# Optimization experiments

Measured on AMD Instinct MI355X. Metric: run time of the kernel, lower is better.

## Reference

```python
import jax, jax.numpy as jnp
import numpy as np

MARGIN = 0.2
ENCODER_STRIDE = 320


def setup_inputs() -> dict:
    key = jax.random.key(0)
    k1, k2, k3, k4 = jax.random.split(key, 4)
    B, D, T, NC = 8, 512, 2048, 4096
    student_features = jax.random.normal(k1, (B, D, T), dtype=jnp.float32)
    codebook = jax.random.normal(k2, (NC, D), dtype=jnp.float32)
    teacher_codes = jax.random.randint(k3, (B, T), 0, NC, dtype=jnp.int64)
    lengths = jax.random.randint(k4, (B,), 0, T * ENCODER_STRIDE, dtype=jnp.int64)
    return {
        "student_features": student_features,
        "teacher_codes": teacher_codes,
        "codebook": codebook,
        "lengths": lengths,
    }


def reference(student_features, teacher_codes, codebook, lengths):
    B, D, T = student_features.shape
    # frame-level valid mask: (B, T)
    frame_lengths = lengths // ENCODER_STRIDE
    mask = (jnp.arange(T)[None, :] < frame_lengths[:, None]).astype(student_features.dtype)

    # (B*T, D) flattened student vectors
    z = jnp.transpose(student_features, (0, 2, 1)).reshape(-1, D)

    # Euclidean cdist via ||z||^2 + ||c||^2 - 2 z c^T (matmul form, like torch.cdist)
    sq = (
        jnp.sum(z * z, axis=-1, keepdims=True)
        + jnp.sum(codebook * codebook, axis=-1)[None, :]
        - 2.0 * jnp.einsum("nd,cd->nc", z, codebook)
    )
    dists = jnp.sqrt(jnp.maximum(sq, 1e-12))  # (B*T, num_codes)

    teacher_flat = teacher_codes.reshape(-1)
    rows = jnp.arange(teacher_flat.shape[0])
    pos_dist = dists[rows, teacher_flat]
    # exclude the target code, then min over codebook
    dists_for_neg = dists.at[rows, teacher_flat].set(jnp.inf)
    neg_dist = jnp.min(dists_for_neg, axis=1)

    triplet = jax.nn.relu(pos_dist.reshape(B, T) - neg_dist.reshape(B, T) + MARGIN)
    loss = jnp.sum(triplet * mask) / (jnp.sum(mask) + 1e-8)
    return loss
```

## Files before the change

### kernel.cpp

```cpp
#include <hip/hip_runtime.h>
#include <hip/hip_bf16.h>

typedef __bf16 bf16x8 __attribute__((ext_vector_type(8)));
typedef float f32x4 __attribute__((ext_vector_type(4)));
typedef int v8i __attribute__((ext_vector_type(8)));

#define NB 8
#define ND 512
#define NT 2048
#define NCODES 4096
#define NM (NB * NT)
#define MARGIN_F 0.2f
#define ENC_STRIDE 320


static __device__ inline unsigned short f2bf(float v) {
    __hip_bfloat16 h = __float2bfloat16(v);
    return __builtin_bit_cast(unsigned short, h);
}

static __device__ inline void async_copy16(const void* g, void* l) {
    __builtin_amdgcn_global_load_lds(
        (const __attribute__((address_space(1))) unsigned int*)g,
        (__attribute__((address_space(3))) unsigned int*)l, 16, 0, 0);
}

__global__ void prep_fused(const float* __restrict__ sf, const float* __restrict__ cb,
                           unsigned char* __restrict__ Zq, unsigned short* __restrict__ Zrm,
                           unsigned char* __restrict__ Cq, float* __restrict__ cnorm) {
    __shared__ float tile[128][65];
    __shared__ float redc[4][16];
    const int tid = threadIdx.x;
    const int wave = tid >> 6, lane = tid & 63, l15 = lane & 15, kq = lane >> 4;

    if (blockIdx.x < 1024) {
        const int bx = blockIdx.x;
        const int t0 = (bx & 31) * 64;
        const int d0 = ((bx >> 5) & 3) * 128;
        const int b = bx >> 7;
        const float* src = sf + (size_t)b * ND * NT;
#pragma unroll
        for (int it = 0; it < 8; it++) {
            int idx = it * 256 + tid;
            int d = idx >> 4, t4 = (idx & 15) * 4;
            float4 v = *(const float4*)(src + (size_t)(d0 + d) * NT + t0 + t4);
            tile[d][t4] = v.x; tile[d][t4 + 1] = v.y; tile[d][t4 + 2] = v.z; tile[d][t4 + 3] = v.w;
        }
        __syncthreads();
        const int m0 = b * NT + t0;
        {
            const int trow = wave * 16 + l15;
            unsigned char q[32];
#pragma unroll
            for (int j = 0; j < 32; j += 2) {
                float a = tile[kq * 32 + j][trow];
                float c = tile[kq * 32 + j + 1][trow];
                int p = __builtin_amdgcn_cvt_pk_fp8_f32(a, c, 0, false);
                q[j] = (unsigned char)(p & 0xFF);
                q[j + 1] = (unsigned char)((p >> 8) & 0xFF);
            }
            const int M_ = m0 >> 7, rg = ((m0 >> 4) & 7) + wave, K_ = d0 >> 7;
            char* base = (char*)Zq + ((size_t)((M_ * 4 + K_) * 8 + rg)) * 2048;
            *(uint4*)(base + lane * 16) = *(uint4*)&q[0];
            *(uint4*)(base + 1024 + lane * 16) = *(uint4*)&q[16];
        }
        {
            int t = tid >> 2;
#pragma unroll
            for (int it = 0; it < 8; it++) {
                int d = (tid & 3) * 4 + it * 16;
                ushort4 o;
                o.x = f2bf(tile[d][t]); o.y = f2bf(tile[d + 1][t]);
                o.z = f2bf(tile[d + 2][t]); o.w = f2bf(tile[d + 3][t]);
                *(ushort4*)(Zrm + (size_t)(m0 + t) * ND + d0 + d) = o;
            }
        }
    } else {
        const int r0 = (blockIdx.x - 1024) * 16;
        const int row = r0 + l15;
        const int K_ = wave;
        const float* src = cb + (size_t)row * ND + K_ * 128 + kq * 32;
        unsigned char q[32];
        float s = 0.0f;
#pragma unroll
        for (int j4 = 0; j4 < 8; j4++) {
            float4 v = *(const float4*)(src + j4 * 4);
            s += v.x * v.x + v.y * v.y + v.z * v.z + v.w * v.w;
            int p0 = __builtin_amdgcn_cvt_pk_fp8_f32(v.x, v.y, 0, false);
            int p1 = __builtin_amdgcn_cvt_pk_fp8_f32(v.z, v.w, 0, false);
            q[j4 * 4 + 0] = (unsigned char)(p0 & 0xFF);
            q[j4 * 4 + 1] = (unsigned char)((p0 >> 8) & 0xFF);
            q[j4 * 4 + 2] = (unsigned char)(p1 & 0xFF);
            q[j4 * 4 + 3] = (unsigned char)((p1 >> 8) & 0xFF);
        }
        const int N_ = r0 >> 7, rg = (r0 >> 4) & 7;
        char* base = (char*)Cq + ((size_t)((N_ * 4 + K_) * 8 + rg)) * 2048;
        *(uint4*)(base + lane * 16) = *(uint4*)&q[0];
        *(uint4*)(base + 1024 + lane * 16) = *(uint4*)&q[16];
        s += __shfl_xor(s, 16);
        s += __shfl_xor(s, 32);
        if (lane < 16) redc[wave][l15] = s;
        __syncthreads();
        if (tid < 16) cnorm[r0 + tid] = redc[0][tid] + redc[1][tid] + redc[2][tid] + redc[3][tid];
    }
}

__global__ __launch_bounds__(256, 2) void triplet_main(
    const unsigned char* __restrict__ Zq, const unsigned char* __restrict__ Cq,
    const float* __restrict__ cnorm, const int* __restrict__ teacher,
    unsigned int* __restrict__ minq) {
    __shared__ __align__(16) unsigned char As[16384];
    __shared__ __align__(16) unsigned char Bs[16384];

    const int M_ = blockIdx.x;
    const int nq = blockIdx.y;
    const int m0 = M_ * 128;
    const int tid = threadIdx.x;
    const int wave = tid >> 6, lane = tid & 63;
    const int wr = wave >> 1, wc = wave & 1;
    const int l15 = lane & 15, quad = lane >> 4;

    unsigned int minu[4][4];
    int tch[4][4];
#pragma unroll
    for (int mi = 0; mi < 4; mi++)
#pragma unroll
        for (int r = 0; r < 4; r++) {
            minu[mi][r] = 0xFFFFFFFFu;
            tch[mi][r] = teacher[m0 + wr * 64 + mi * 16 + quad * 4 + r];
        }

    const char* gA0 = (const char*)Zq + (size_t)M_ * 4 * 16384 + wave * 4096 + lane * 16;
    char* lA = (char*)As + wave * 4096;
    char* lB = (char*)Bs + wave * 4096;

    for (int nt = 0; nt < 4; nt++) {
        const int N_ = nq * 4 + nt;
        const int n0 = N_ * 128;
        const char* gA = gA0;
        const char* gB = (const char*)Cq + (size_t)N_ * 4 * 16384 + wave * 4096 + lane * 16;
        f32x4 acc[4][4] = {};

        for (int kt = 0; kt < 4; kt++) {
#pragma unroll
            for (int i = 0; i < 4; i++) {
                async_copy16(gA + i * 1024, lA + i * 1024);
                async_copy16(gB + i * 1024, lB + i * 1024);
            }
            gA += 16384; gB += 16384;
            __syncthreads();

            v8i av[4], bv[4];
#pragma unroll
            for (int mi = 0; mi < 4; mi++) {
                int rg = wr * 4 + mi;
                union { uint4 q[2]; v8i v; } u;
                u.q[0] = *(const uint4*)(As + rg * 2048 + lane * 16);
                u.q[1] = *(const uint4*)(As + rg * 2048 + 1024 + lane * 16);
                av[mi] = u.v;
            }
#pragma unroll
            for (int ni = 0; ni < 4; ni++) {
                int rg = wc * 4 + ni;
                union { uint4 q[2]; v8i v; } u;
                u.q[0] = *(const uint4*)(Bs + rg * 2048 + lane * 16);
                u.q[1] = *(const uint4*)(Bs + rg * 2048 + 1024 + lane * 16);
                bv[ni] = u.v;
            }
#pragma unroll
            for (int mi = 0; mi < 4; mi++)
#pragma unroll
                for (int ni = 0; ni < 4; ni++)
                    acc[mi][ni] = __builtin_amdgcn_mfma_scale_f32_16x16x128_f8f6f4(
                        av[mi], bv[ni], acc[mi][ni], 0, 0,
                        0, 0x7F7F7F7F, 0, 0x7F7F7F7F);
            __syncthreads();
        }

        float cn[4]; int col[4];
#pragma unroll
        for (int ni = 0; ni < 4; ni++) {
            col[ni] = n0 + wc * 64 + ni * 16 + l15;
            cn[ni] = cnorm[col[ni]];
        }
#pragma unroll
        for (int mi = 0; mi < 4; mi++)
#pragma unroll
            for (int r = 0; r < 4; r++) {
                int t = tch[mi][r];
#pragma unroll
                for (int ni = 0; ni < 4; ni++) {
                    float val = fmaxf(fmaf(-2.0f, acc[mi][ni][r], cn[ni]), 0.0f);
                    unsigned int u = (__builtin_bit_cast(unsigned int, val) & 0xFFFFF000u)
                                     | (unsigned int)col[ni];
                    u = (col[ni] == t) ? 0xFFFFFFFFu : u;
                    minu[mi][r] = min(minu[mi][r], u);
                }
            }
    }

    const int slot = nq * 2 + wc;
#pragma unroll
    for (int mi = 0; mi < 4; mi++)
#pragma unroll
        for (int r = 0; r < 4; r++) {
            unsigned int u = minu[mi][r];
#pragma unroll
            for (int off = 1; off < 16; off <<= 1) u = min(u, (unsigned int)__shfl_xor((int)u, off));
            if (l15 == 0) {
                int m = m0 + wr * 64 + mi * 16 + quad * 4 + r;
                minq[(size_t)slot * NM + m] = u;
            }
        }
}

__global__ void refine(const unsigned short* __restrict__ Zrm, const float* __restrict__ cb,
                       const unsigned int* __restrict__ minq, const int* __restrict__ teacher,
                       const int* __restrict__ lengths, float* __restrict__ blocksums) {
    const int tid = threadIdx.x, wave = tid >> 6, lane = tid & 63;
    const int m = blockIdx.x * 4 + wave;
    unsigned int u = minq[(size_t)(lane & 15) * NM + m];
    u = min(u, (unsigned int)__shfl_xor((int)u, 1));
    u = min(u, (unsigned int)__shfl_xor((int)u, 2));
    u = min(u, (unsigned int)__shfl_xor((int)u, 4));
    u = min(u, (unsigned int)__shfl_xor((int)u, 8));
    const int ng = (int)(u & 0xFFFu);
    const int tch = teacher[m];
    bf16x8 z8 = *(const bf16x8*)(Zrm + (size_t)m * ND + lane * 8);
    const float* cn_ = cb + (size_t)ng * ND + lane * 8;
    const float* ct_ = cb + (size_t)tch * ND + lane * 8;
    float an = 0.0f, at = 0.0f;
#pragma unroll
    for (int i = 0; i < 2; i++) {
        float4 vn = *(const float4*)(cn_ + i * 4);
        float4 vt = *(const float4*)(ct_ + i * 4);
        float z0 = (float)z8[i * 4 + 0], z1 = (float)z8[i * 4 + 1];
        float z2 = (float)z8[i * 4 + 2], z3 = (float)z8[i * 4 + 3];
        float d;
        d = z0 - vn.x; an += d * d;  d = z0 - vt.x; at += d * d;
        d = z1 - vn.y; an += d * d;  d = z1 - vt.y; at += d * d;
        d = z2 - vn.z; an += d * d;  d = z2 - vt.z; at += d * d;
        d = z3 - vn.w; an += d * d;  d = z3 - vt.w; at += d * d;
    }
#pragma unroll
    for (int off = 1; off < 64; off <<= 1) {
        an += __shfl_xor(an, off);
        at += __shfl_xor(at, off);
    }
    __shared__ float red[4];
    if (lane == 0) {
        float negd = sqrtf(fmaxf(an, 1e-12f));
        float posd = sqrtf(fmaxf(at, 1e-12f));
        float tri = fmaxf(posd - negd + MARGIN_F, 0.0f);
        int t = m & (NT - 1);
        int b = m >> 11;
        int flen = lengths[b] / ENC_STRIDE;
        red[wave] = (t < flen) ? tri : 0.0f;
    }
    __syncthreads();
    if (tid == 0) blocksums[blockIdx.x] = red[0] + red[1] + red[2] + red[3];
}

__global__ void finalize(const float* __restrict__ blocksums, const int* __restrict__ lengths,
                         float* __restrict__ out) {
    int tid = threadIdx.x;
    float s = 0.0f;
#pragma unroll
    for (int i = 0; i < 16; i++) s += blocksums[tid + i * 256];
#pragma unroll
    for (int off = 1; off < 64; off <<= 1) s += __shfl_xor(s, off);
    __shared__ float red[4];
    int lane = tid & 63, w = tid >> 6;
    if (lane == 0) red[w] = s;
    __syncthreads();
    if (tid == 0) {
        float cnt = 0.0f;
        for (int b = 0; b < NB; b++) cnt += (float)(lengths[b] / ENC_STRIDE);
        out[0] = (red[0] + red[1] + red[2] + red[3]) / (cnt + 1e-8f);
    }
}

extern "C" void kernel_launch(void* const* d_in, const int* in_sizes, int n_in,
                              void* d_out, int out_size, void* d_ws, size_t ws_size,
                              hipStream_t stream) {
    const float* sf = (const float*)d_in[0];
    const int* teacher = (const int*)d_in[1];
    const float* cb = (const float*)d_in[2];
    const int* lengths = (const int*)d_in[3];

    char* ws = (char*)d_ws;
    unsigned char* Zq = (unsigned char*)(ws);
    unsigned char* Cq = (unsigned char*)(ws + 8388608);
    unsigned short* Zrm = (unsigned short*)(ws + 10485760);
    float* cnorm = (float*)(ws + 27262976);
    unsigned int* minq = (unsigned int*)(ws + 27279360);
    float* blocksums = (float*)(ws + 28327936);

    prep_fused<<<1280, 256, 0, stream>>>(sf, cb, Zq, Zrm, Cq, cnorm);
    triplet_main<<<dim3(128, 8), 256, 0, stream>>>(Zq, Cq, cnorm, teacher, minq);
    refine<<<NM / 4, 256, 0, stream>>>(Zrm, cb, minq, teacher, lengths, blocksums);
    finalize<<<1, 256, 0, stream>>>(blocksums, lengths, (float*)d_out);
}
```

Before: 147.1 us.

## Double-buffer LDS tiles in triplet_main with flattened prefetch loop

Doubles the A and B shared-memory buffers and flattens the nt/kt loops into 16 steps. Each step first prefetches the next K-tile with async global-to-LDS copies into the other buffer, then runs MFMAs on the current one, so global load latency overlaps with compute. It also drops one of the two barriers per step. The cost is twice the LDS per block, which could limit occupancy, and the epilogue min-reduction now sits inside the pipelined loop.

```diff
diff --git a/kernel.cpp b/kernel.cpp
--- a/kernel.cpp
+++ b/kernel.cpp
@@ -109,8 +109,8 @@
     const unsigned char* __restrict__ Zq, const unsigned char* __restrict__ Cq,
     const float* __restrict__ cnorm, const int* __restrict__ teacher,
     unsigned int* __restrict__ minq) {
-    __shared__ __align__(16) unsigned char As[16384];
-    __shared__ __align__(16) unsigned char Bs[16384];
+    __shared__ __align__(16) unsigned char As[2][16384];
+    __shared__ __align__(16) unsigned char Bs[2][16384];
 
     const int M_ = blockIdx.x;
     const int nq = blockIdx.y;
@@ -130,73 +130,96 @@
             tch[mi][r] = teacher[m0 + wr * 64 + mi * 16 + quad * 4 + r];
         }
 
-    const char* gA0 = (const char*)Zq + (size_t)M_ * 4 * 16384 + wave * 4096 + lane * 16;
-    char* lA = (char*)As + wave * 4096;
-    char* lB = (char*)Bs + wave * 4096;
-
-    for (int nt = 0; nt < 4; nt++) {
-        const int N_ = nq * 4 + nt;
-        const int n0 = N_ * 128;
-        const char* gA = gA0;
-        const char* gB = (const char*)Cq + (size_t)N_ * 4 * 16384 + wave * 4096 + lane * 16;
-        f32x4 acc[4][4] = {};
-
-        for (int kt = 0; kt < 4; kt++) {
+    const char* gA0 = (const char*)Zq + (size_t)M_ * 65536 + wave * 4096 + lane * 16;
+    const char* gB0 = (const char*)Cq + (size_t)(nq * 4) * 65536 + wave * 4096 + lane * 16;
+
+    {
+        char* lA = (char*)As[0] + wave * 4096;
+        char* lB = (char*)Bs[0] + wave * 4096;
+#pragma unroll
+        for (int i = 0; i < 4; i++) {
+            async_copy16(gA0 + i * 1024, lA + i * 1024);
+            async_copy16(gB0 + i * 1024, lB + i * 1024);
+        }
+    }
+
+    f32x4 acc[4][4];
+
+    for (int s = 0; s < 16; s++) {
+        __syncthreads();
+
+        if (s < 15) {
+            int sn = s + 1;
+            int ktn = sn & 3, ntn = sn >> 2;
+            const char* gA = gA0 + ktn * 16384;
+            const char* gB = gB0 + (size_t)ntn * 65536 + ktn * 16384;
+            char* lA = (char*)As[sn & 1] + wave * 4096;
+            char* lB = (char*)Bs[sn & 1] + wave * 4096;
 #pragma unroll
             for (int i = 0; i < 4; i++) {
                 async_copy16(gA + i * 1024, lA + i * 1024);
                 async_copy16(gB + i * 1024, lB + i * 1024);
             }
-            gA += 16384; gB += 16384;
-            __syncthreads();
-
-            v8i av[4], bv[4];
-#pragma unroll
-            for (int mi = 0; mi < 4; mi++) {
-                int rg = wr * 4 + mi;
-                union { uint4 q[2]; v8i v; } u;
-                u.q[0] = *(const uint4*)(As + rg * 2048 + lane * 16);
-                u.q[1] = *(const uint4*)(As + rg * 2048 + 1024 + lane * 16);
-                av[mi] = u.v;
-            }
+        }
+
+        if ((s & 3) == 0) {
+#pragma unroll
+            for (int mi = 0; mi < 4; mi++)
+#pragma unroll
+                for (int ni = 0; ni < 4; ni++) acc[mi][ni] = (f32x4){0.f, 0.f, 0.f, 0.f};
+        }
+
+        const unsigned char* bufA = As[s & 1];
+        const unsigned char* bufB = Bs[s & 1];
+        v8i av[4], bv[4];
+#pragma unroll
+        for (int mi = 0; mi < 4; mi++) {
+            int rg = wr * 4 + mi;
+            union { uint4 q[2]; v8i v; } u;
+            u.q[0] = *(const uint4*)(bufA + rg * 2048 + lane * 16);
+            u.q[1] = *(const uint4*)(bufA + rg * 2048 + 1024 + lane * 16);
+            av[mi] = u.v;
+        }
+#pragma unroll
+        for (int ni = 0; ni < 4; ni++) {
+            int rg = wc * 4 + ni;
+            union { uint4 q[2]; v8i v; } u;
+            u.q[0] = *(const uint4*)(bufB + rg * 2048 + lane * 16);
+            u.q[1] = *(const uint4*)(bufB + rg * 2048 + 1024 + lane * 16);
+            bv[ni] = u.v;
+        }
+#pragma unroll
+        for (int mi = 0; mi < 4; mi++)
+#pragma unroll
+            for (int ni = 0; ni < 4; ni++)
+                acc[mi][ni] = __builtin_amdgcn_mfma_scale_f32_16x16x128_f8f6f4(
+                    av[mi], bv[ni], acc[mi][ni], 0, 0,
+                    0, 0x7F7F7F7F, 0, 0x7F7F7F7F);
+
+        if ((s & 3) == 3) {
+            const int nt = s >> 2;
+            const int n0 = (nq * 4 + nt) * 128;
+            float cn[4]; int col[4];
 #pragma unroll
             for (int ni = 0; ni < 4; ni++) {
-                int rg = wc * 4 + ni;
-                union { uint4 q[2]; v8i v; } u;
-                u.q[0] = *(const uint4*)(Bs + rg * 2048 + lane * 16);
-                u.q[1] = *(const uint4*)(Bs + rg * 2048 + 1024 + lane * 16);
-                bv[ni] = u.v;
+                col[ni] = n0 + wc * 64 + ni * 16 + l15;
+                cn[ni] = cnorm[col[ni]];
             }
 #pragma unroll
             for (int mi = 0; mi < 4; mi++)
 #pragma unroll
-                for (int ni = 0; ni < 4; ni++)
-                    acc[mi][ni] = __builtin_amdgcn_mfma_scale_f32_16x16x128_f8f6f4(
-                        av[mi], bv[ni], acc[mi][ni], 0, 0,
-                        0, 0x7F7F7F7F, 0, 0x7F7F7F7F);
-            __syncthreads();
-        }
-
-        float cn[4]; int col[4];
-#pragma unroll
-        for (int ni = 0; ni < 4; ni++) {
-            col[ni] = n0 + wc * 64 + ni * 16 + l15;
-            cn[ni] = cnorm[col[ni]];
-        }
-#pragma unroll
-        for (int mi = 0; mi < 4; mi++)
-#pragma unroll
-            for (int r = 0; r < 4; r++) {
-                int t = tch[mi][r];
-#pragma unroll
-                for (int ni = 0; ni < 4; ni++) {
-                    float val = fmaxf(fmaf(-2.0f, acc[mi][ni][r], cn[ni]), 0.0f);
-                    unsigned int u = (__builtin_bit_cast(unsigned int, val) & 0xFFFFF000u)
-                                     | (unsigned int)col[ni];
-                    u = (col[ni] == t) ? 0xFFFFFFFFu : u;
-                    minu[mi][r] = min(minu[mi][r], u);
+                for (int r = 0; r < 4; r++) {
+                    int t = tch[mi][r];
+#pragma unroll
+                    for (int ni = 0; ni < 4; ni++) {
+                        float val = fmaxf(fmaf(-2.0f, acc[mi][ni][r], cn[ni]), 0.0f);
+                        unsigned int u = (__builtin_bit_cast(unsigned int, val) & 0xFFFFF000u)
+                                         | (unsigned int)col[ni];
+                        u = (col[ni] == t) ? 0xFFFFFFFFu : u;
+                        minu[mi][r] = min(minu[mi][r], u);
+                    }
                 }
-            }
+        }
     }
 
     const int slot = nq * 2 + wc;
```

New measurement: 148.1 us. Within noise of the previous version (+0.7%).

## Keep full A tile resident in LDS and stream B fragments directly from global

Applied to the files above, without the earlier changes.

The whole 128x512 fp8 Z tile (64KB) is loaded into LDS once per block rather than once per N tile and K step. The codebook operand is now read straight from global memory into registers in two halves per K step. This removes the per-iteration __syncthreads barriers and the redundant re-staging of A. In exchange each block needs 64KB of LDS, which may cut occupancy below the launch bound of 2 blocks per CU. B loads also go through global/L2 latency with little software pipelining.

```diff
diff --git a/kernel.cpp b/kernel.cpp
--- a/kernel.cpp
+++ b/kernel.cpp
@@ -109,8 +109,7 @@
     const unsigned char* __restrict__ Zq, const unsigned char* __restrict__ Cq,
     const float* __restrict__ cnorm, const int* __restrict__ teacher,
     unsigned int* __restrict__ minq) {
-    __shared__ __align__(16) unsigned char As[16384];
-    __shared__ __align__(16) unsigned char Bs[16384];
+    __shared__ __align__(16) unsigned char As[65536];
 
     const int M_ = blockIdx.x;
     const int nq = blockIdx.y;
@@ -120,6 +119,13 @@
     const int wr = wave >> 1, wc = wave & 1;
     const int l15 = lane & 15, quad = lane >> 4;
 
+    {
+        const char* gA = (const char*)Zq + (size_t)M_ * 65536 + wave * 16384 + lane * 16;
+        char* lA = (char*)As + wave * 16384;
+#pragma unroll
+        for (int i = 0; i < 16; i++) async_copy16(gA + i * 1024, lA + i * 1024);
+    }
+
     unsigned int minu[4][4];
     int tch[4][4];
 #pragma unroll
@@ -129,52 +135,50 @@
             minu[mi][r] = 0xFFFFFFFFu;
             tch[mi][r] = teacher[m0 + wr * 64 + mi * 16 + quad * 4 + r];
         }
-
-    const char* gA0 = (const char*)Zq + (size_t)M_ * 4 * 16384 + wave * 4096 + lane * 16;
-    char* lA = (char*)As + wave * 4096;
-    char* lB = (char*)Bs + wave * 4096;
+    __syncthreads();
 
     for (int nt = 0; nt < 4; nt++) {
         const int N_ = nq * 4 + nt;
         const int n0 = N_ * 128;
-        const char* gA = gA0;
-        const char* gB = (const char*)Cq + (size_t)N_ * 4 * 16384 + wave * 4096 + lane * 16;
+        const char* gB = (const char*)Cq + (size_t)N_ * 65536 + (wc * 4) * 2048 + lane * 16;
         f32x4 acc[4][4] = {};
 
         for (int kt = 0; kt < 4; kt++) {
-#pragma unroll
-            for (int i = 0; i < 4; i++) {
-                async_copy16(gA + i * 1024, lA + i * 1024);
-                async_copy16(gB + i * 1024, lB + i * 1024);
-            }
-            gA += 16384; gB += 16384;
-            __syncthreads();
-
-            v8i av[4], bv[4];
+            const char* gBk = gB + kt * 16384;
+            const unsigned char* aB = As + (kt * 8 + wr * 4) * 2048 + lane * 16;
+
+            union { uint4 q[2]; v8i v; } b0, b1;
+            b0.q[0] = *(const uint4*)(gBk);
+            b0.q[1] = *(const uint4*)(gBk + 1024);
+            b1.q[0] = *(const uint4*)(gBk + 2048);
+            b1.q[1] = *(const uint4*)(gBk + 3072);
+
+            v8i av[4];
 #pragma unroll
             for (int mi = 0; mi < 4; mi++) {
-                int rg = wr * 4 + mi;
                 union { uint4 q[2]; v8i v; } u;
-                u.q[0] = *(const uint4*)(As + rg * 2048 + lane * 16);
-                u.q[1] = *(const uint4*)(As + rg * 2048 + 1024 + lane * 16);
+                u.q[0] = *(const uint4*)(aB + mi * 2048);
+                u.q[1] = *(const uint4*)(aB + mi * 2048 + 1024);
                 av[mi] = u.v;
             }
 #pragma unroll
-            for (int ni = 0; ni < 4; ni++) {
-                int rg = wc * 4 + ni;
-                union { uint4 q[2]; v8i v; } u;
-                u.q[0] = *(const uint4*)(Bs + rg * 2048 + lane * 16);
-                u.q[1] = *(const uint4*)(Bs + rg * 2048 + 1024 + lane * 16);
-                bv[ni] = u.v;
-            }
-#pragma unroll
-            for (int mi = 0; mi < 4; mi++)
-#pragma unroll
-                for (int ni = 0; ni < 4; ni++)
-                    acc[mi][ni] = __builtin_amdgcn_mfma_scale_f32_16x16x128_f8f6f4(
-                        av[mi], bv[ni], acc[mi][ni], 0, 0,
-                        0, 0x7F7F7F7F, 0, 0x7F7F7F7F);
-            __syncthreads();
+            for (int mi = 0; mi < 4; mi++) {
+                acc[mi][0] = __builtin_amdgcn_mfma_scale_f32_16x16x128_f8f6f4(
+                    av[mi], b0.v, acc[mi][0], 0, 0, 0, 0x7F7F7F7F, 0, 0x7F7F7F7F);
+                acc[mi][1] = __builtin_amdgcn_mfma_scale_f32_16x16x128_f8f6f4(
+                    av[mi], b1.v, acc[mi][1], 0, 0, 0, 0x7F7F7F7F, 0, 0x7F7F7F7F);
+            }
+            b0.q[0] = *(const uint4*)(gBk + 4096);
+            b0.q[1] = *(const uint4*)(gBk + 5120);
+            b1.q[0] = *(const uint4*)(gBk + 6144);
+            b1.q[1] = *(const uint4*)(gBk + 7168);
+#pragma unroll
+            for (int mi = 0; mi < 4; mi++) {
+                acc[mi][2] = __builtin_amdgcn_mfma_scale_f32_16x16x128_f8f6f4(
+                    av[mi], b0.v, acc[mi][2], 0, 0, 0, 0x7F7F7F7F, 0, 0x7F7F7F7F);
+                acc[mi][3] = __builtin_amdgcn_mfma_scale_f32_16x16x128_f8f6f4(
+                    av[mi], b1.v, acc[mi][3], 0, 0, 0, 0x7F7F7F7F, 0, 0x7F7F7F7F);
+            }
         }
 
         float cn[4]; int col[4];
```

Result: slower. 157.2 us (+6.8%).

## Drop exact refine pass; compute distances directly from FP8 GEMM plus row norms

Applied to the files above, without the earlier changes.

Removes the bf16 row-major copy of the features and the refine kernel that recomputed exact distances to the chosen negative and the teacher code. Instead the main GEMM kernel tracks both the minimum non-target value and the target value in float, and the prep kernel writes partial squared norms of each frame. A light reduction kernel combines these into the final distances. This cuts the extra write of the feature copy and the gather of codebook rows, but the loss now relies entirely on FP8-precision dot products, which may lose accuracy.

```diff
diff --git a/kernel.cpp b/kernel.cpp
--- a/kernel.cpp
+++ b/kernel.cpp
@@ -1,7 +1,6 @@
 #include <hip/hip_runtime.h>
 #include <hip/hip_bf16.h>
 
-typedef __bf16 bf16x8 __attribute__((ext_vector_type(8)));
 typedef float f32x4 __attribute__((ext_vector_type(4)));
 typedef int v8i __attribute__((ext_vector_type(8)));
 
@@ -14,11 +13,6 @@
 #define ENC_STRIDE 320
 
 
-static __device__ inline unsigned short f2bf(float v) {
-    __hip_bfloat16 h = __float2bfloat16(v);
-    return __builtin_bit_cast(unsigned short, h);
-}
-
 static __device__ inline void async_copy16(const void* g, void* l) {
     __builtin_amdgcn_global_load_lds(
         (const __attribute__((address_space(1))) unsigned int*)g,
@@ -26,7 +20,7 @@
 }
 
 __global__ void prep_fused(const float* __restrict__ sf, const float* __restrict__ cb,
-                           unsigned char* __restrict__ Zq, unsigned short* __restrict__ Zrm,
+                           unsigned char* __restrict__ Zq, float* __restrict__ npart,
                            unsigned char* __restrict__ Cq, float* __restrict__ cnorm) {
     __shared__ float tile[128][65];
     __shared__ float redc[4][16];
@@ -64,16 +58,14 @@
             *(uint4*)(base + lane * 16) = *(uint4*)&q[0];
             *(uint4*)(base + 1024 + lane * 16) = *(uint4*)&q[16];
         }
-        {
-            int t = tid >> 2;
-#pragma unroll
-            for (int it = 0; it < 8; it++) {
-                int d = (tid & 3) * 4 + it * 16;
-                ushort4 o;
-                o.x = f2bf(tile[d][t]); o.y = f2bf(tile[d + 1][t]);
-                o.z = f2bf(tile[d + 2][t]); o.w = f2bf(tile[d + 3][t]);
-                *(ushort4*)(Zrm + (size_t)(m0 + t) * ND + d0 + d) = o;
-            }
+        if (tid < 64) {
+            float s = 0.0f;
+#pragma unroll 16
+            for (int d = 0; d < 128; d++) {
+                float v = tile[d][tid];
+                s += v * v;
+            }
+            npart[(size_t)(d0 >> 7) * NM + m0 + tid] = s;
         }
     } else {
         const int r0 = (blockIdx.x - 1024) * 16;
@@ -108,7 +100,7 @@
 __global__ __launch_bounds__(256, 2) void triplet_main(
     const unsigned char* __restrict__ Zq, const unsigned char* __restrict__ Cq,
     const float* __restrict__ cnorm, const int* __restrict__ teacher,
-    unsigned int* __restrict__ minq) {
+    float* __restrict__ negq, float* __restrict__ posq) {
     __shared__ __align__(16) unsigned char As[16384];
     __shared__ __align__(16) unsigned char Bs[16384];
 
@@ -120,13 +112,15 @@
     const int wr = wave >> 1, wc = wave & 1;
     const int l15 = lane & 15, quad = lane >> 4;
 
-    unsigned int minu[4][4];
+    const float INF = __builtin_inff();
+    float minv[4][4], posv[4][4];
     int tch[4][4];
 #pragma unroll
     for (int mi = 0; mi < 4; mi++)
 #pragma unroll
         for (int r = 0; r < 4; r++) {
-            minu[mi][r] = 0xFFFFFFFFu;
+            minv[mi][r] = INF;
+            posv[mi][r] = INF;
             tch[mi][r] = teacher[m0 + wr * 64 + mi * 16 + quad * 4 + r];
         }
 
@@ -190,11 +184,10 @@
                 int t = tch[mi][r];
 #pragma unroll
                 for (int ni = 0; ni < 4; ni++) {
-                    float val = fmaxf(fmaf(-2.0f, acc[mi][ni][r], cn[ni]), 0.0f);
-                    unsigned int u = (__builtin_bit_cast(unsigned int, val) & 0xFFFFF000u)
-                                     | (unsigned int)col[ni];
-                    u = (col[ni] == t) ? 0xFFFFFFFFu : u;
-                    minu[mi][r] = min(minu[mi][r], u);
+                    float val = fmaf(-2.0f, acc[mi][ni][r], cn[ni]);
+                    bool ist = (col[ni] == t);
+                    minv[mi][r] = fminf(minv[mi][r], ist ? INF : val);
+                    posv[mi][r] = fminf(posv[mi][r], ist ? val : INF);
                 }
             }
     }
@@ -204,79 +197,58 @@
     for (int mi = 0; mi < 4; mi++)
 #pragma unroll
         for (int r = 0; r < 4; r++) {
-            unsigned int u = minu[mi][r];
-#pragma unroll
-            for (int off = 1; off < 16; off <<= 1) u = min(u, (unsigned int)__shfl_xor((int)u, off));
+            float mn = minv[mi][r], ps = posv[mi][r];
+#pragma unroll
+            for (int off = 1; off < 16; off <<= 1) {
+                mn = fminf(mn, __shfl_xor(mn, off));
+                ps = fminf(ps, __shfl_xor(ps, off));
+            }
             if (l15 == 0) {
                 int m = m0 + wr * 64 + mi * 16 + quad * 4 + r;
-                minq[(size_t)slot * NM + m] = u;
-            }
-        }
-}
-
-__global__ void refine(const unsigned short* __restrict__ Zrm, const float* __restrict__ cb,
-                       const unsigned int* __restrict__ minq, const int* __restrict__ teacher,
-                       const int* __restrict__ lengths, float* __restrict__ blocksums) {
-    const int tid = threadIdx.x, wave = tid >> 6, lane = tid & 63;
-    const int m = blockIdx.x * 4 + wave;
-    unsigned int u = minq[(size_t)(lane & 15) * NM + m];
-    u = min(u, (unsigned int)__shfl_xor((int)u, 1));
-    u = min(u, (unsigned int)__shfl_xor((int)u, 2));
-    u = min(u, (unsigned int)__shfl_xor((int)u, 4));
-    u = min(u, (unsigned int)__shfl_xor((int)u, 8));
-    const int ng = (int)(u & 0xFFFu);
-    const int tch = teacher[m];
-    bf16x8 z8 = *(const bf16x8*)(Zrm + (size_t)m * ND + lane * 8);
-    const float* cn_ = cb + (size_t)ng * ND + lane * 8;
-    const float* ct_ = cb + (size_t)tch * ND + lane * 8;
-    float an = 0.0f, at = 0.0f;
-#pragma unroll
-    for (int i = 0; i < 2; i++) {
-        float4 vn = *(const float4*)(cn_ + i * 4);
-        float4 vt = *(const float4*)(ct_ + i * 4);
-        float z0 = (float)z8[i * 4 + 0], z1 = (float)z8[i * 4 + 1];
-        float z2 = (float)z8[i * 4 + 2], z3 = (float)z8[i * 4 + 3];
-        float d;
-        d = z0 - vn.x; an += d * d;  d = z0 - vt.x; at += d * d;
-        d = z1 - vn.y; an += d * d;  d = z1 - vt.y; at += d * d;
-        d = z2 - vn.z; an += d * d;  d = z2 - vt.z; at += d * d;
-        d = z3 - vn.w; an += d * d;  d = z3 - vt.w; at += d * d;
-    }
-#pragma unroll
-    for (int off = 1; off < 64; off <<= 1) {
-        an += __shfl_xor(an, off);
-        at += __shfl_xor(at, off);
-    }
+                negq[(size_t)slot * NM + m] = mn;
+                posq[(size_t)slot * NM + m] = ps;
+            }
+        }
+}
+
+__global__ void reduce_rows(const float* __restrict__ negq, const float* __restrict__ posq,
+                            const float* __restrict__ npart, const int* __restrict__ lengths,
+                            float* __restrict__ blocksums) {
+    const float INF = __builtin_inff();
+    const int m = blockIdx.x * 256 + threadIdx.x;
+    float mn = INF, ps = INF;
+#pragma unroll
+    for (int s = 0; s < 16; s++) {
+        mn = fminf(mn, negq[(size_t)s * NM + m]);
+        ps = fminf(ps, posq[(size_t)s * NM + m]);
+    }
+    float zn = npart[m] + npart[NM + m] + npart[2 * NM + m] + npart[3 * NM + m];
+    float negd = sqrtf(fmaxf(zn + mn, 1e-12f));
+    float posd = sqrtf(fmaxf(zn + ps, 1e-12f));
+    float tri = fmaxf(posd - negd + MARGIN_F, 0.0f);
+    int b = m >> 11;
+    int tt = m & (NT - 1);
+    int flen = lengths[b] / ENC_STRIDE;
+    float val = (tt < flen) ? tri : 0.0f;
+
     __shared__ float red[4];
-    if (lane == 0) {
-        float negd = sqrtf(fmaxf(an, 1e-12f));
-        float posd = sqrtf(fmaxf(at, 1e-12f));
-        float tri = fmaxf(posd - negd + MARGIN_F, 0.0f);
-        int t = m & (NT - 1);
-        int b = m >> 11;
-        int flen = lengths[b] / ENC_STRIDE;
-        red[wave] = (t < flen) ? tri : 0.0f;
-    }
+#pragma unroll
+    for (int off = 1; off < 64; off <<= 1) val += __shfl_xor(val, off);
+    int lane = threadIdx.x & 63, w = threadIdx.x >> 6;
+    if (lane == 0) red[w] = val;
     __syncthreads();
-    if (tid == 0) blocksums[blockIdx.x] = red[0] + red[1] + red[2] + red[3];
+    if (threadIdx.x == 0) blocksums[blockIdx.x] = red[0] + red[1] + red[2] + red[3];
 }
 
 __global__ void finalize(const float* __restrict__ blocksums, const int* __restrict__ lengths,
                          float* __restrict__ out) {
-    int tid = threadIdx.x;
-    float s = 0.0f;
-#pragma unroll
-    for (int i = 0; i < 16; i++) s += blocksums[tid + i * 256];
+    float s = blocksums[threadIdx.x];
 #pragma unroll
     for (int off = 1; off < 64; off <<= 1) s += __shfl_xor(s, off);
-    __shared__ float red[4];
-    int lane = tid & 63, w = tid >> 6;
-    if (lane == 0) red[w] = s;
-    __syncthreads();
-    if (tid == 0) {
+    if (threadIdx.x == 0) {
         float cnt = 0.0f;
         for (int b = 0; b < NB; b++) cnt += (float)(lengths[b] / ENC_STRIDE);
-        out[0] = (red[0] + red[1] + red[2] + red[3]) / (cnt + 1e-8f);
+        out[0] = s / (cnt + 1e-8f);
     }
 }
 
@@ -291,13 +263,14 @@
     char* ws = (char*)d_ws;
     unsigned char* Zq = (unsigned char*)(ws);
     unsigned char* Cq = (unsigned char*)(ws + 8388608);
-    unsigned short* Zrm = (unsigned short*)(ws + 10485760);
-    float* cnorm = (float*)(ws + 27262976);
-    unsigned int* minq = (unsigned int*)(ws + 27279360);
-    float* blocksums = (float*)(ws + 28327936);
-
-    prep_fused<<<1280, 256, 0, stream>>>(sf, cb, Zq, Zrm, Cq, cnorm);
-    triplet_main<<<dim3(128, 8), 256, 0, stream>>>(Zq, Cq, cnorm, teacher, minq);
-    refine<<<NM / 4, 256, 0, stream>>>(Zrm, cb, minq, teacher, lengths, blocksums);
-    finalize<<<1, 256, 0, stream>>>(blocksums, lengths, (float*)d_out);
-}
+    float* cnorm = (float*)(ws + 10485760);
+    float* npart = (float*)(ws + 10502144);
+    float* negq = (float*)(ws + 10764288);
+    float* posq = (float*)(ws + 11812864);
+    float* blocksums = (float*)(ws + 12861440);
+
+    prep_fused<<<1280, 256, 0, stream>>>(sf, cb, Zq, npart, Cq, cnorm);
+    triplet_main<<<dim3(128, 8), 256, 0, stream>>>(Zq, Cq, cnorm, teacher, negq, posq);
+    reduce_rows<<<NM / 256, 256, 0, stream>>>(negq, posq, npart, lengths, blocksums);
+    finalize<<<1, 64, 0, stream>>>(blocksums, lengths, (float*)d_out);
+}
```

After: 134.4 us. 8.6% less time.
